# Kernel optimization log

Measured on AMD Instinct MI355X. Metric: run time of the kernel, lower is better.

## Reference

```python
import jax, jax.numpy as jnp
import numpy as np

B, S = 4, 1024           # sequences, tokens per sequence (prefill)
H, HKV, D = 32, 8, 128   # q heads, kv heads (GQA), head_dim
HID = H * D              # 4096
THETA = 10000.0


def setup_inputs() -> dict:
    key = jax.random.key(0)
    k1, k2, k3 = jax.random.split(key, 3)
    T = B * S
    hidden_states = jax.random.normal(k1, (T, HID), jnp.float32) * 0.02
    w_qkv = jax.random.normal(k2, ((H + 2 * HKV) * D, HID), jnp.float32) * 0.02
    w_dense = jax.random.normal(k3, (HID, HID), jnp.float32) * 0.02
    positions = jnp.tile(jnp.arange(S, dtype=jnp.int32), B)  # per-token position ids
    return {"positions": positions, "hidden_states": hidden_states,
            "w_qkv": w_qkv, "w_dense": w_dense}


def _rope(x, positions):
    # NeoX-style rotary embedding (vLLM rotary_dim == head_dim). x: [T, n_heads, D]
    half = D // 2
    inv_freq = 1.0 / (THETA ** (jnp.arange(half, dtype=jnp.float32) / half))
    freqs = positions.astype(jnp.float32)[:, None] * inv_freq       # [T, half]
    cos = jnp.cos(freqs)[:, None, :]
    sin = jnp.sin(freqs)[:, None, :]
    x1, x2 = x[..., :half], x[..., half:]
    return jnp.concatenate([x1 * cos - x2 * sin, x2 * cos + x1 * sin], axis=-1)


def reference(positions, hidden_states, w_qkv, w_dense):
    T = hidden_states.shape[0]
    scale = 1.0 / np.sqrt(D)
    # fused QKV projection (bias=False in config)
    qkv = hidden_states @ w_qkv.T                                   # [T, (H+2*HKV)*D]
    q, k, v = jnp.split(qkv, [H * D, (H + HKV) * D], axis=-1)
    q = q.reshape(T, H, D)
    k = k.reshape(T, HKV, D)
    v = v.reshape(T, HKV, D)
    # fused RoPE on q and k
    q = _rope(q, positions)
    k = _rope(k, positions)
    # causal GQA attention over each sequence
    G = H // HKV
    q = q.reshape(B, S, HKV, G, D)
    k = k.reshape(B, S, HKV, D)
    v = v.reshape(B, S, HKV, D)
    scores = jnp.einsum('bshgd,bthd->bhgst', q, k) * scale          # [B,HKV,G,S,S]
    causal = jnp.tril(jnp.ones((S, S), dtype=bool))
    scores = jnp.where(causal, scores, jnp.finfo(scores.dtype).min)
    probs = jax.nn.softmax(scores, axis=-1)
    attn = jnp.einsum('bhgst,bthd->bshgd', probs, v)                # [B,S,HKV,G,D]
    attn = attn.reshape(T, HID)
    # output projection (skip_bias_add, bias=False -> output only)
    return attn @ w_dense.T
```

## Files before the change

### kernel.cpp

```cpp
#include <hip/hip_runtime.h>

typedef short bf16x8 __attribute__((ext_vector_type(8)));
typedef float f32x4 __attribute__((ext_vector_type(4)));

__device__ __forceinline__ ushort f2bf(float f) {
  union { float f; unsigned u; } x; x.f = f;
  unsigned r = x.u + 0x7fffu + ((x.u >> 16) & 1u);
  return (ushort)(r >> 16);
}
__device__ __forceinline__ float bf2f(ushort u) {
  union { unsigned u; float f; } x; x.u = ((unsigned)u) << 16; return x.f;
}
__device__ __forceinline__ void load_lds16(const void* g, void* l) {
  __builtin_amdgcn_global_load_lds((const __attribute__((address_space(1))) void*)g,
                                   (__attribute__((address_space(3))) void*)l, 16, 0, 0);
}
typedef __attribute__((address_space(3))) const ushort* lds_cp;
__device__ __forceinline__ bf16x8 dsr16(const ushort* p) {
  bf16x8 r;
  asm volatile("ds_read_b128 %0, %1" : "=v"(r) : "v"((lds_cp)p));
  return r;
}
__device__ __forceinline__ void store_out(float* p, float v) { *p = v; }
__device__ __forceinline__ void store_out(ushort* p, float v) { *p = f2bf(v); }

__global__ __launch_bounds__(256) void cast_kernel(const float* __restrict__ in,
                                                   ushort* __restrict__ out, int n4) {
  int i = blockIdx.x * 256 + threadIdx.x;
  if (i < n4) {
    float4 v = ((const float4*)in)[i];
    ushort4 o;
    o.x = f2bf(v.x); o.y = f2bf(v.y); o.z = f2bf(v.z); o.w = f2bf(v.w);
    ((ushort4*)out)[i] = o;
  }
}

#define PBAR() do { asm volatile("" ::: "memory"); __builtin_amdgcn_s_barrier(); \
                    asm volatile("" ::: "memory"); } while (0)
#define WAITK(n) do { asm volatile("s_waitcnt lgkmcnt(" #n ")" ::: "memory"); \
                      __builtin_amdgcn_sched_barrier(0); } while (0)

template <typename OutT>
__global__ __launch_bounds__(512) void gemm256(const ushort* __restrict__ A,
                                               const ushort* __restrict__ B,
                                               OutT* __restrict__ C,
                                               int M, int N, int K) {
  __shared__ ushort As[2][256 * 64];
  __shared__ ushort Bs[2][256 * 64];
  const int tid = threadIdx.x;
  const int wave = tid >> 6, lane = tid & 63;
  const int quad = lane >> 4, lx = lane & 15;
  const int wr = wave >> 2, wc = wave & 3;
  const int m0 = blockIdx.y * 256, n0 = blockIdx.x * 256;
  const int NT = K >> 6;
  const int sgrow = lane >> 3;
  const int sgchunk = ((lane & 7) ^ sgrow) * 8;

  f32x4 acc[8][4] = {};
  bf16x8 afA[4], afB[4], bfA[4], bfB[4];

#define STAGE_A(T, H)                                                         \
  do {                                                                        \
    _Pragma("unroll") for (int i_ = 0; i_ < 2; ++i_) {                        \
      const int rg_ = (H) * 128 + wave * 16 + i_ * 8;                         \
      load_lds16(A + (size_t)(m0 + rg_ + sgrow) * K + (T) * 64 + sgchunk,     \
                 &As[(T) & 1][rg_ * 64]);                                     \
    }                                                                         \
  } while (0)
#define STAGE_B(T, H)                                                         \
  do {                                                                        \
    _Pragma("unroll") for (int i_ = 0; i_ < 2; ++i_) {                        \
      const int rg_ = (H) * 128 + wave * 16 + i_ * 8;                         \
      load_lds16(B + (size_t)(n0 + rg_ + sgrow) * K + (T) * 64 + sgchunk,     \
                 &Bs[(T) & 1][rg_ * 64]);                                     \
    }                                                                         \
  } while (0)
#define READ_AF(dst, QM, S)                                                   \
  _Pragma("unroll") for (int mm = 0; mm < 4; ++mm)                            \
    dst[mm] = dsr16(curA + (wr * 128 + ((QM) * 4 + mm) * 16 + lx) * 64        \
                    + ((((S) * 4 + quad) ^ (lx & 7)) * 8));
#define READ_BF(dst, S)                                                       \
  _Pragma("unroll") for (int nn = 0; nn < 4; ++nn)                            \
    dst[nn] = dsr16(curB + (wc * 64 + nn * 16 + lx) * 64                      \
                    + ((((S) * 4 + quad) ^ (lx & 7)) * 8));
#define MFMA16(M0, av, bv)                                                    \
  __builtin_amdgcn_s_setprio(1);                                              \
  _Pragma("unroll") for (int mm = 0; mm < 4; ++mm)                            \
  _Pragma("unroll") for (int nn = 0; nn < 4; ++nn)                            \
    acc[(M0) + mm][nn] = __builtin_amdgcn_mfma_f32_16x16x32_bf16(             \
        av[mm], bv[nn], acc[(M0) + mm][nn], 0, 0, 0);                         \
  __builtin_amdgcn_s_setprio(0);

  STAGE_A(0, 0); STAGE_A(0, 1); STAGE_B(0, 0); STAGE_B(0, 1);
  if (NT > 1) { STAGE_B(1, 0); STAGE_B(1, 1); }

  for (int t = 0; t < NT; ++t) {
    asm volatile("" ::: "memory");
    if (t == NT - 1) { asm volatile("s_waitcnt vmcnt(0)" ::: "memory"); }
    else             { asm volatile("s_waitcnt vmcnt(4)" ::: "memory"); }
    __builtin_amdgcn_s_barrier();
    asm volatile("" ::: "memory");
    const ushort* curA = As[t & 1];
    const ushort* curB = Bs[t & 1];

    READ_AF(afA, 0, 0); READ_BF(bfA, 0);
    READ_AF(afB, 1, 0);
    if (t + 1 < NT) { STAGE_A(t + 1, 0); STAGE_A(t + 1, 1); }
    WAITK(4);
    MFMA16(0, afA, bfA);
    READ_AF(afA, 0, 1); READ_BF(bfB, 1);
    WAITK(8);
    MFMA16(4, afB, bfA);
    READ_AF(afB, 1, 1);
    WAITK(4);
    PBAR();
    if (t + 2 < NT) { STAGE_B(t + 2, 0); STAGE_B(t + 2, 1); }
    MFMA16(0, afA, bfB);
    WAITK(0);
    MFMA16(4, afB, bfB);
  }

#pragma unroll
  for (int m = 0; m < 8; ++m)
#pragma unroll
    for (int n = 0; n < 4; ++n)
#pragma unroll
      for (int r = 0; r < 4; ++r) {
        const int row = m0 + wr * 128 + m * 16 + quad * 4 + r;
        const int col = n0 + wc * 64 + n * 16 + lx;
        store_out(C + (size_t)row * N + col, acc[m][n][r]);
      }
#undef STAGE_A
#undef STAGE_B
#undef READ_AF
#undef READ_BF
#undef MFMA16
}

__global__ __launch_bounds__(256) void rope_kernel(const int* __restrict__ pos,
                                                   ushort* __restrict__ qkv) {
  const int rid = blockIdx.x * 4 + (threadIdx.x >> 6);
  const int d = threadIdx.x & 63;
  const int t = rid / 40;
  const int hh = rid - t * 40;
  ushort* p = qkv + (size_t)t * 6144 + (hh < 32 ? hh * 128 : 4096 + (hh - 32) * 128);
  const float inv_freq = powf(10000.0f, -(float)d * (1.0f / 64.0f));
  const float fr = (float)pos[t] * inv_freq;
  float sn, cs;
  sincosf(fr, &sn, &cs);
  const float x1 = bf2f(p[d]);
  const float x2 = bf2f(p[d + 64]);
  p[d] = f2bf(x1 * cs - x2 * sn);
  p[d + 64] = f2bf(x2 * cs + x1 * sn);
}

__global__ __launch_bounds__(256) void attn_fused(const ushort* __restrict__ qkv,
                                                  ushort* __restrict__ outb) {
  const int bid = blockIdx.x;
  const int pair = bid & 7;
  const int h = (bid >> 3) & 31;
  const int b = bid >> 8;
  const int kvh = h >> 2;
  const int tid = threadIdx.x, wave = tid >> 6, lane = tid & 63;
  const int quad = lane >> 4, lx = lane & 15;

  __shared__ ushort Ks[64 * 128];
  __shared__ ushort Vt[128 * 64];
  __shared__ ushort Ps[64 * 64];

  const size_t tb = (size_t)b * 1024;
  const float scale = 0.08838834764831843f;

#pragma unroll
  for (int phase = 0; phase < 2; ++phase) {
    const int qt64 = phase ? (15 - pair) : pair;
    const int qrow0 = qt64 * 64 + wave * 16;

    bf16x8 qf[4];
#pragma unroll
    for (int ks = 0; ks < 4; ++ks)
      qf[ks] = *(const bf16x8*)(qkv + (tb + qrow0 + lx) * 6144 + h * 128 + ks * 32 + quad * 8);

    f32x4 o[8] = {};
    float mst[4], lst[4];
#pragma unroll
    for (int r = 0; r < 4; ++r) { mst[r] = -1e30f; lst[r] = 0.f; }

    const int nkt = qt64 + 1;
    for (int it = 0; it < nkt; ++it) {
      const int kb = it * 64;
      __syncthreads();
#pragma unroll
      for (int i = 0; i < 4; ++i) {
        const int rg = wave * 16 + i * 4;
        const int row = rg + quad;
        load_lds16(qkv + (tb + kb + row) * 6144 + 4096 + kvh * 128 + ((lx ^ (row & 7)) * 8),
                   Ks + rg * 128);
      }
      {
        const ushort* vp = qkv + (tb + kb + lane) * 6144 + 5120 + kvh * 128 + wave * 32;
#pragma unroll
        for (int c = 0; c < 4; ++c) {
          bf16x8 v8 = *(const bf16x8*)(vp + c * 8);
#pragma unroll
          for (int e = 0; e < 8; ++e) {
            const int d = wave * 32 + c * 8 + e;
            Vt[d * 64 + (((lane >> 3) ^ (d & 7)) * 8) + (lane & 7)] = (ushort)v8[e];
          }
        }
      }
      __syncthreads();

      f32x4 s[4] = {};
#pragma unroll
      for (int ks = 0; ks < 4; ++ks) {
        bf16x8 kf[4];
#pragma unroll
        for (int kt = 0; kt < 4; ++kt)
          kf[kt] = *(const bf16x8*)(Ks + (kt * 16 + lx) * 128 + (((ks * 4 + quad) ^ (lx & 7)) * 8));
#pragma unroll
        for (int kt = 0; kt < 4; ++kt)
          s[kt] = __builtin_amdgcn_mfma_f32_16x16x32_bf16(qf[ks], kf[kt], s[kt], 0, 0, 0);
      }

      const bool diag = (kb + 63 > qrow0);
#pragma unroll
      for (int r = 0; r < 4; ++r) {
        const int row = qrow0 + quad * 4 + r;
        float mx = -1e30f;
#pragma unroll
        for (int kt = 0; kt < 4; ++kt) {
          float sv = s[kt][r] * scale;
          if (diag && (kb + kt * 16 + lx > row)) sv = -1e30f;
          s[kt][r] = sv;
          mx = fmaxf(mx, sv);
        }
        mx = fmaxf(mx, __shfl_xor(mx, 1));
        mx = fmaxf(mx, __shfl_xor(mx, 2));
        mx = fmaxf(mx, __shfl_xor(mx, 4));
        mx = fmaxf(mx, __shfl_xor(mx, 8));
        const float mnew = fmaxf(mst[r], mx);
        const float alpha = __expf(mst[r] - mnew);
        mst[r] = mnew;
        float rs = 0.f;
#pragma unroll
        for (int kt = 0; kt < 4; ++kt) {
          const float pv = __expf(s[kt][r] - mnew);
          s[kt][r] = pv;
          rs += pv;
        }
        rs += __shfl_xor(rs, 1); rs += __shfl_xor(rs, 2);
        rs += __shfl_xor(rs, 4); rs += __shfl_xor(rs, 8);
        lst[r] = lst[r] * alpha + rs;
#pragma unroll
        for (int dt = 0; dt < 8; ++dt) o[dt][r] *= alpha;
        const int prow = wave * 16 + quad * 4 + r;
#pragma unroll
        for (int kt = 0; kt < 4; ++kt)
          Ps[prow * 64 + (((kt * 2 + (lx >> 3)) ^ (prow & 7)) * 8) + (lx & 7)] = f2bf(s[kt][r]);
      }
      __syncthreads();

#pragma unroll
      for (int ks2 = 0; ks2 < 2; ++ks2) {
        const int prow = wave * 16 + lx;
        bf16x8 pf = *(const bf16x8*)(Ps + prow * 64 + (((ks2 * 4 + quad) ^ (lx & 7)) * 8));
#pragma unroll
        for (int dt = 0; dt < 8; ++dt) {
          bf16x8 vf = *(const bf16x8*)(Vt + (dt * 16 + lx) * 64 + (((ks2 * 4 + quad) ^ (lx & 7)) * 8));
          o[dt] = __builtin_amdgcn_mfma_f32_16x16x32_bf16(pf, vf, o[dt], 0, 0, 0);
        }
      }
    }

#pragma unroll
    for (int r = 0; r < 4; ++r) {
      const float inv = 1.f / lst[r];
      const int row = qrow0 + quad * 4 + r;
#pragma unroll
      for (int dt = 0; dt < 8; ++dt)
        outb[(tb + row) * 4096 + h * 128 + dt * 16 + lx] = f2bf(o[dt][r] * inv);
    }
  }
}

extern "C" void kernel_launch(void* const* d_in, const int* in_sizes, int n_in,
                              void* d_out, int out_size, void* d_ws, size_t ws_size,
                              hipStream_t stream) {
  const int* positions = (const int*)d_in[0];
  const float* hidden  = (const float*)d_in[1];
  const float* w_qkv   = (const float*)d_in[2];
  const float* w_dense = (const float*)d_in[3];
  float* out = (float*)d_out;

  ushort* hidden_bf = (ushort*)d_ws;
  ushort* wqkv_bf   = hidden_bf + (size_t)16777216;
  ushort* wdense_bf = wqkv_bf   + (size_t)25165824;
  ushort* qkv_bf    = wdense_bf + (size_t)16777216;
  ushort* attn_bf   = qkv_bf    + (size_t)25165824;

  cast_kernel<<<16384, 256, 0, stream>>>(hidden,  hidden_bf, 4194304);
  cast_kernel<<<24576, 256, 0, stream>>>(w_qkv,   wqkv_bf,   6291456);
  cast_kernel<<<16384, 256, 0, stream>>>(w_dense, wdense_bf, 4194304);

  gemm256<ushort><<<dim3(24, 16), 512, 0, stream>>>(hidden_bf, wqkv_bf, qkv_bf, 4096, 6144, 4096);

  rope_kernel<<<40960, 256, 0, stream>>>(positions, qkv_bf);

  attn_fused<<<1024, 256, 0, stream>>>(qkv_bf, attn_bf);

  gemm256<float><<<dim3(16, 16), 512, 0, stream>>>(attn_bf, wdense_bf, out, 4096, 4096, 4096);
}
```

Baseline: 759.4 us.

## Pre-transpose V into a global buffer and stage it with async LDS loads

Adds a separate kernel that transposes V once per batch and kv-head into a [d][key] global layout. The attention kernel then fills its transposed V tile with direct global-to-LDS loads using an XOR swizzle, replacing the per-element scattered LDS writes repeated in every block. The extra kernel launch and memory pass cost less work than before because each V tile is reused by many query heads and tiles. The transposed buffer reuses the hidden-state workspace, which is no longer needed after the QKV GEMM. RoPE also replaces powf with exp2f to compute the inverse frequency.

New measurement: 704.5 us. 1.08x faster.

```diff
diff --git a/kernel.cpp b/kernel.cpp
--- a/kernel.cpp
+++ b/kernel.cpp
@@ -144,7 +144,7 @@
   const int t = rid / 40;
   const int hh = rid - t * 40;
   ushort* p = qkv + (size_t)t * 6144 + (hh < 32 ? hh * 128 : 4096 + (hh - 32) * 128);
-  const float inv_freq = powf(10000.0f, -(float)d * (1.0f / 64.0f));
+  const float inv_freq = exp2f((float)d * -0.20762050593046f);
   const float fr = (float)pos[t] * inv_freq;
   float sn, cs;
   sincosf(fr, &sn, &cs);
@@ -154,7 +154,35 @@
   p[d + 64] = f2bf(x2 * cs + x1 * sn);
 }
 
+__global__ __launch_bounds__(256) void vtrans_kernel(const ushort* __restrict__ qkv,
+                                                     ushort* __restrict__ vtg) {
+  __shared__ ushort T[64][136];
+  const int kt = blockIdx.x, bh = blockIdx.y;
+  const int b = bh >> 3, kvh = bh & 7;
+  const int t = threadIdx.x;
+  const size_t tb = (size_t)b * 1024;
+  const int kb = kt * 64;
+#pragma unroll
+  for (int i = 0; i < 4; ++i) {
+    const int c = i * 256 + t;
+    const int key = c >> 4, d0 = (c & 15) * 8;
+    *(bf16x8*)&T[key][d0] =
+        *(const bf16x8*)(qkv + (tb + kb + key) * 6144 + 5120 + kvh * 128 + d0);
+  }
+  __syncthreads();
+  const int d = t >> 1, half = t & 1;
+#pragma unroll
+  for (int j = 0; j < 4; ++j) {
+    const int k0 = half * 32 + j * 8;
+    bf16x8 v;
+#pragma unroll
+    for (int e = 0; e < 8; ++e) v[e] = (short)T[k0 + e][d];
+    *(bf16x8*)(vtg + ((size_t)bh * 128 + d) * 1024 + kb + k0) = v;
+  }
+}
+
 __global__ __launch_bounds__(256) void attn_fused(const ushort* __restrict__ qkv,
+                                                  const ushort* __restrict__ vtg,
                                                   ushort* __restrict__ outb) {
   const int bid = blockIdx.x;
   const int pair = bid & 7;
@@ -169,6 +197,7 @@
   __shared__ ushort Ps[64 * 64];
 
   const size_t tb = (size_t)b * 1024;
+  const ushort* vbase = vtg + (size_t)(b * 8 + kvh) * 131072;
   const float scale = 0.08838834764831843f;
 
 #pragma unroll
@@ -197,17 +226,12 @@
         load_lds16(qkv + (tb + kb + row) * 6144 + 4096 + kvh * 128 + ((lx ^ (row & 7)) * 8),
                    Ks + rg * 128);
       }
-      {
-        const ushort* vp = qkv + (tb + kb + lane) * 6144 + 5120 + kvh * 128 + wave * 32;
-#pragma unroll
-        for (int c = 0; c < 4; ++c) {
-          bf16x8 v8 = *(const bf16x8*)(vp + c * 8);
-#pragma unroll
-          for (int e = 0; e < 8; ++e) {
-            const int d = wave * 32 + c * 8 + e;
-            Vt[d * 64 + (((lane >> 3) ^ (d & 7)) * 8) + (lane & 7)] = (ushort)v8[e];
-          }
-        }
+#pragma unroll
+      for (int i = 0; i < 4; ++i) {
+        const int rg = wave * 32 + i * 8;
+        const int row = rg + (lane >> 3);
+        load_lds16(vbase + (size_t)row * 1024 + kb + (((lane & 7) ^ (row & 7)) * 8),
+                   Vt + rg * 64);
       }
       __syncthreads();
 
@@ -298,6 +322,7 @@
   ushort* wdense_bf = wqkv_bf   + (size_t)25165824;
   ushort* qkv_bf    = wdense_bf + (size_t)16777216;
   ushort* attn_bf   = qkv_bf    + (size_t)25165824;
+  ushort* vt_g      = hidden_bf;
 
   cast_kernel<<<16384, 256, 0, stream>>>(hidden,  hidden_bf, 4194304);
   cast_kernel<<<24576, 256, 0, stream>>>(w_qkv,   wqkv_bf,   6291456);
@@ -307,7 +332,9 @@
 
   rope_kernel<<<40960, 256, 0, stream>>>(positions, qkv_bf);
 
-  attn_fused<<<1024, 256, 0, stream>>>(qkv_bf, attn_bf);
+  vtrans_kernel<<<dim3(16, 32), 256, 0, stream>>>(qkv_bf, vt_g);
+
+  attn_fused<<<1024, 256, 0, stream>>>(qkv_bf, vt_g, attn_bf);
 
   gemm256<float><<<dim3(16, 16), 512, 0, stream>>>(attn_bf, wdense_bf, out, 4096, 4096, 4096);
 }
```
